# Optimization experiments

Measured on AMD Instinct MI355X. Metric: run time of the kernel, lower is better.

## Reference

```python
import jax, jax.numpy as jnp
import numpy as np

C_RATIO, T_RATIO = 0.8, 0.9

def _mlp(v, w1, w2):
    # v: [b, n]; w1: [hid, n]; w2: [n, hid]  (1x1x1 convs on pooled vector == matmuls)
    return jnp.einsum('nh,bh->bn', w2, jax.nn.relu(jnp.einsum('hn,bn->bh', w1, v)))

def _wta(x, ratio):
    # winner-take-all along last dim: keep top ceil(ratio*n) entries, zero the rest
    k = int(np.ceil(ratio * x.shape[-1]))
    thr = jax.lax.top_k(x, k)[0][..., -1:]
    mask = (x >= thr).astype(x.dtype)
    return x * mask, mask

def setup_inputs() -> dict:
    key = jax.random.key(0)
    ks = jax.random.split(key, 5)
    b, f, c, h, w = 16, 8, 256, 32, 32
    x = jax.random.normal(ks[0], (b, f, c, h, w), jnp.float32)
    ta_w1 = jax.random.normal(ks[1], (f, f), jnp.float32) * 0.3   # TimeAttention conv1 (reduction=1)
    ta_w2 = jax.random.normal(ks[2], (f, f), jnp.float32) * 0.3   # TimeAttention conv2
    ca_w1 = jax.random.normal(ks[3], (c, c), jnp.float32) * 0.06  # ChannelAttention conv1
    ca_w2 = jax.random.normal(ks[4], (c, c), jnp.float32) * 0.06  # ChannelAttention conv2
    return {"x": x, "ta_w1": ta_w1, "ta_w2": ta_w2, "ca_w1": ca_w1, "ca_w2": ca_w2}

def reference(x, ta_w1, ta_w2, ca_w1, ca_w2):
    # TimeAttention: global avg/max pool over (c,h,w) -> [b,f], shared MLP, sigmoid
    t_avg = x.mean(axis=(2, 3, 4))
    t_max = x.max(axis=(2, 3, 4))
    ta = jax.nn.sigmoid(_mlp(t_avg, ta_w1, ta_w2) + _mlp(t_max, ta_w1, ta_w2))  # [b,f]
    out = x * ta[:, :, None, None, None]
    # ChannelAttention on ta*x: pool over (f,h,w) -> [b,c]
    c_avg = out.mean(axis=(1, 3, 4))
    c_max = out.max(axis=(1, 3, 4))
    ca = jax.nn.sigmoid(_mlp(c_avg, ca_w1, ca_w2) + _mlp(c_max, ca_w1, ca_w2))  # [b,c]
    # winner-take-all saliency masking
    sal_c, mask_c = _wta(ca, C_RATIO)   # [b,c]
    sal_t, mask_t = _wta(ta, T_RATIO)   # [b,f]
    coef = (sal_t[:, :, None] * sal_c[:, None, :])[..., None, None]   # [b,f,c,1,1]
    mask = (mask_t[:, :, None] * mask_c[:, None, :])[..., None, None]
    return x * mask * coef
```

## Files before the change

kernel.cpp:

```cpp
#include <hip/hip_runtime.h>
#include <math.h>

#define B 16
#define F 8
#define C 256
#define HW 1024
#define NROWS (B*F*C)
#define KC 205

typedef float f4 __attribute__((ext_vector_type(4)));

__global__ __launch_bounds__(256) void k_rowstat(const float* __restrict__ x,
                                                 float* __restrict__ sums,
                                                 float* __restrict__ maxs) {
    const int wave = threadIdx.x >> 6;
    const int lane = threadIdx.x & 63;
    const int row  = blockIdx.x * 4 + wave;
    const float* p = x + (size_t)row * HW;

    float s = 0.f, m = -INFINITY;
#pragma unroll
    for (int k = 0; k < 4; ++k) {
        float4 v = *reinterpret_cast<const float4*>(p + k * 256 + lane * 4);
        s += (v.x + v.y) + (v.z + v.w);
        m = fmaxf(m, fmaxf(fmaxf(v.x, v.y), fmaxf(v.z, v.w)));
    }
#pragma unroll
    for (int off = 32; off > 0; off >>= 1) {
        s += __shfl_down(s, off);
        m = fmaxf(m, __shfl_down(m, off));
    }
    if (lane == 0) { sums[row] = s; maxs[row] = m; }
}

__global__ __launch_bounds__(256) void k_att(const float* __restrict__ sums,
                                             const float* __restrict__ maxs,
                                             const float* __restrict__ tw1,
                                             const float* __restrict__ tw2,
                                             const float* __restrict__ w1,
                                             const float* __restrict__ w2,
                                             float* __restrict__ srow) {
    __shared__ float tavg[F], tmx[F], th[F], ta_s[F];
    __shared__ float vavg[C], vmax[C], hsum[C], ca[C];
    const int b    = blockIdx.x;
    const int t    = threadIdx.x;
    const int wave = t >> 6;
    const int lane = t & 63;

    for (int f = wave; f < F; f += 4) {
        const float* sp = sums + (b * F + f) * C;
        const float* mp = maxs + (b * F + f) * C;
        float s = (sp[lane] + sp[lane + 64]) + (sp[lane + 128] + sp[lane + 192]);
        float m = fmaxf(fmaxf(mp[lane], mp[lane + 64]),
                        fmaxf(mp[lane + 128], mp[lane + 192]));
#pragma unroll
        for (int off = 32; off > 0; off >>= 1) {
            s += __shfl_down(s, off);
            m = fmaxf(m, __shfl_down(m, off));
        }
        if (lane == 0) { tavg[f] = s * (1.f / (float)(C * HW)); tmx[f] = m; }
    }
    __syncthreads();

    if (t < F) {
        float ha = 0.f, hm = 0.f;
        for (int n = 0; n < F; ++n) {
            float w = tw1[t * F + n];
            ha += w * tavg[n];
            hm += w * tmx[n];
        }
        th[t] = fmaxf(ha, 0.f) + fmaxf(hm, 0.f);
    }
    __syncthreads();
    if (t < F) {
        float o = 0.f;
        for (int h = 0; h < F; ++h) o += tw2[t * F + h] * th[h];
        ta_s[t] = 1.f / (1.f + expf(-o));
    }
    __syncthreads();

    {
        float s = 0.f, m = -INFINITY;
        for (int f = 0; f < F; ++f) {
            float w = ta_s[f];
            s += w * sums[(b * F + f) * C + t];
            m = fmaxf(m, w * maxs[(b * F + f) * C + t]);
        }
        vavg[t] = s * (1.f / (float)(F * HW));
        vmax[t] = m;
    }
    __syncthreads();

    {
        float ha = 0.f, hm = 0.f;
        const float* w1r = w1 + t * C;
        for (int n = 0; n < C; ++n) {
            float w = w1r[n];
            ha += w * vavg[n];
            hm += w * vmax[n];
        }
        hsum[t] = fmaxf(ha, 0.f) + fmaxf(hm, 0.f);
    }
    __syncthreads();

    float cav;
    {
        float o = 0.f;
        const float* w2r = w2 + t * C;
        for (int h = 0; h < C; ++h) o += w2r[h] * hsum[h];
        cav = 1.f / (1.f + expf(-o));
        ca[t] = cav;
    }
    __syncthreads();

    int rank = 0;
    for (int j = 0; j < C; ++j) rank += (ca[j] > cav);
    float sc = (rank < KC) ? cav : 0.f;
    for (int f = 0; f < F; ++f)
        srow[b * (F * C) + f * C + t] = ta_s[f] * sc;
}

__global__ __launch_bounds__(256) void k_scale(const float* __restrict__ x,
                                               const float* __restrict__ srow,
                                               float* __restrict__ out,
                                               int n4) {
    int idx = blockIdx.x * blockDim.x + threadIdx.x;
    const int stride = gridDim.x * blockDim.x;
    for (int i = idx; i < n4; i += stride) {
        f4 v = reinterpret_cast<const f4*>(x)[i];
        float sc = srow[i >> 8];
        v *= sc;
        __builtin_nontemporal_store(v, reinterpret_cast<f4*>(out) + i);
    }
}

extern "C" void kernel_launch(void* const* d_in, const int* in_sizes, int n_in,
                              void* d_out, int out_size, void* d_ws, size_t ws_size,
                              hipStream_t stream) {
    const float* x     = (const float*)d_in[0];
    const float* ta_w1 = (const float*)d_in[1];
    const float* ta_w2 = (const float*)d_in[2];
    const float* ca_w1 = (const float*)d_in[3];
    const float* ca_w2 = (const float*)d_in[4];
    float* out = (float*)d_out;

    float* ws   = (float*)d_ws;
    float* sums = ws;
    float* maxs = ws + NROWS;
    float* srow = ws + 2 * NROWS;

    k_rowstat<<<NROWS / 4, 256, 0, stream>>>(x, sums, maxs);
    k_att<<<B, 256, 0, stream>>>(sums, maxs, ta_w1, ta_w2, ca_w1, ca_w2, srow);
    k_scale<<<2048, 256, 0, stream>>>(x, srow, out, NROWS * HW / 4);
}
```

Baseline: 86.45 us.

## Fuse attention computation into scale kernel and skip loads for masked channels

The attention MLP kernel is merged into the scaling pass. Each of the 2048 blocks recomputes its batch's time and channel attention redundantly and then scales a 16-row chunk, which removes one launch and the srow round trip. Rows whose channel coefficient is zero are written as zeros without reading x, which saves about 20% of the read traffic. The row-stat kernel now has each wave reduce two rows with all eight loads issued up front. In exchange, every block repeats the 256x256 MLP and the O(C^2) ranking, which adds compute ahead of the streaming work.

```diff
diff --git a/kernel.cpp b/kernel.cpp
--- a/kernel.cpp
+++ b/kernel.cpp
@@ -15,37 +15,60 @@
                                                  float* __restrict__ maxs) {
     const int wave = threadIdx.x >> 6;
     const int lane = threadIdx.x & 63;
-    const int row  = blockIdx.x * 4 + wave;
-    const float* p = x + (size_t)row * HW;
+    const int row0 = blockIdx.x * 8 + wave * 2;
+    const float* p0 = x + (size_t)row0 * HW + lane * 4;
+    const float* p1 = p0 + HW;
 
-    float s = 0.f, m = -INFINITY;
-#pragma unroll
-    for (int k = 0; k < 4; ++k) {
-        float4 v = *reinterpret_cast<const float4*>(p + k * 256 + lane * 4);
-        s += (v.x + v.y) + (v.z + v.w);
-        m = fmaxf(m, fmaxf(fmaxf(v.x, v.y), fmaxf(v.z, v.w)));
-    }
+    float4 a0 = *reinterpret_cast<const float4*>(p0);
+    float4 a1 = *reinterpret_cast<const float4*>(p0 + 256);
+    float4 a2 = *reinterpret_cast<const float4*>(p0 + 512);
+    float4 a3 = *reinterpret_cast<const float4*>(p0 + 768);
+    float4 b0 = *reinterpret_cast<const float4*>(p1);
+    float4 b1 = *reinterpret_cast<const float4*>(p1 + 256);
+    float4 b2 = *reinterpret_cast<const float4*>(p1 + 512);
+    float4 b3 = *reinterpret_cast<const float4*>(p1 + 768);
+
+    float s0 = (((a0.x + a0.y) + (a0.z + a0.w)) + ((a1.x + a1.y) + (a1.z + a1.w)))
+             + (((a2.x + a2.y) + (a2.z + a2.w)) + ((a3.x + a3.y) + (a3.z + a3.w)));
+    float m0 = fmaxf(fmaxf(fmaxf(fmaxf(a0.x, a0.y), fmaxf(a0.z, a0.w)),
+                           fmaxf(fmaxf(a1.x, a1.y), fmaxf(a1.z, a1.w))),
+                     fmaxf(fmaxf(fmaxf(a2.x, a2.y), fmaxf(a2.z, a2.w)),
+                           fmaxf(fmaxf(a3.x, a3.y), fmaxf(a3.z, a3.w))));
+    float s1 = (((b0.x + b0.y) + (b0.z + b0.w)) + ((b1.x + b1.y) + (b1.z + b1.w)))
+             + (((b2.x + b2.y) + (b2.z + b2.w)) + ((b3.x + b3.y) + (b3.z + b3.w)));
+    float m1 = fmaxf(fmaxf(fmaxf(fmaxf(b0.x, b0.y), fmaxf(b0.z, b0.w)),
+                           fmaxf(fmaxf(b1.x, b1.y), fmaxf(b1.z, b1.w))),
+                     fmaxf(fmaxf(fmaxf(b2.x, b2.y), fmaxf(b2.z, b2.w)),
+                           fmaxf(fmaxf(b3.x, b3.y), fmaxf(b3.z, b3.w))));
+
 #pragma unroll
     for (int off = 32; off > 0; off >>= 1) {
-        s += __shfl_down(s, off);
-        m = fmaxf(m, __shfl_down(m, off));
+        s0 += __shfl_down(s0, off);
+        m0 = fmaxf(m0, __shfl_down(m0, off));
+        s1 += __shfl_down(s1, off);
+        m1 = fmaxf(m1, __shfl_down(m1, off));
     }
-    if (lane == 0) { sums[row] = s; maxs[row] = m; }
+    if (lane == 0) {
+        sums[row0] = s0; maxs[row0] = m0;
+        sums[row0 + 1] = s1; maxs[row0 + 1] = m1;
+    }
 }
 
-__global__ __launch_bounds__(256) void k_att(const float* __restrict__ sums,
-                                             const float* __restrict__ maxs,
-                                             const float* __restrict__ tw1,
-                                             const float* __restrict__ tw2,
-                                             const float* __restrict__ w1,
-                                             const float* __restrict__ w2,
-                                             float* __restrict__ srow) {
+__global__ __launch_bounds__(256) void k_att_scale(const float* __restrict__ x,
+                                                   const float* __restrict__ sums,
+                                                   const float* __restrict__ maxs,
+                                                   const float* __restrict__ tw1,
+                                                   const float* __restrict__ tw2,
+                                                   const float* __restrict__ w1,
+                                                   const float* __restrict__ w2,
+                                                   float* __restrict__ out) {
     __shared__ float tavg[F], tmx[F], th[F], ta_s[F];
-    __shared__ float vavg[C], vmax[C], hsum[C], ca[C];
-    const int b    = blockIdx.x;
-    const int t    = threadIdx.x;
-    const int wave = t >> 6;
-    const int lane = t & 63;
+    __shared__ float vavg[C], vmax[C], hsum[C], ca[C], sc_s[C];
+    const int b     = blockIdx.x >> 7;
+    const int chunk = blockIdx.x & 127;
+    const int t     = threadIdx.x;
+    const int wave  = t >> 6;
+    const int lane  = t & 63;
 
     for (int f = wave; f < F; f += 4) {
         const float* sp = sums + (b * F + f) * C;
@@ -113,24 +136,30 @@
     }
     __syncthreads();
 
-    int rank = 0;
-    for (int j = 0; j < C; ++j) rank += (ca[j] > cav);
-    float sc = (rank < KC) ? cav : 0.f;
-    for (int f = 0; f < F; ++f)
-        srow[b * (F * C) + f * C + t] = ta_s[f] * sc;
-}
+    {
+        int rank = 0;
+        for (int j = 0; j < C; ++j) rank += (ca[j] > cav);
+        sc_s[t] = (rank < KC) ? cav : 0.f;
+    }
+    __syncthreads();
 
-__global__ __launch_bounds__(256) void k_scale(const float* __restrict__ x,
-                                               const float* __restrict__ srow,
-                                               float* __restrict__ out,
-                                               int n4) {
-    int idx = blockIdx.x * blockDim.x + threadIdx.x;
-    const int stride = gridDim.x * blockDim.x;
-    for (int i = idx; i < n4; i += stride) {
-        f4 v = reinterpret_cast<const f4*>(x)[i];
-        float sc = srow[i >> 8];
-        v *= sc;
-        __builtin_nontemporal_store(v, reinterpret_cast<f4*>(out) + i);
+    const float taf = ta_s[chunk >> 4];
+    const int   c0  = (chunk & 15) * 16;
+    const int base4 = (b * 2048 + chunk * 16) * 256;
+    const f4* x4 = reinterpret_cast<const f4*>(x);
+    f4* o4 = reinterpret_cast<f4*>(out);
+
+    for (int it = 0; it < 16; ++it) {
+        const float scv = sc_s[c0 + it];
+        const int gi = base4 + it * 256 + t;
+        if (scv == 0.f) {
+            f4 z = {0.f, 0.f, 0.f, 0.f};
+            __builtin_nontemporal_store(z, o4 + gi);
+        } else {
+            f4 v = x4[gi];
+            v *= (taf * scv);
+            __builtin_nontemporal_store(v, o4 + gi);
+        }
     }
 }
 
@@ -147,9 +176,8 @@
     float* ws   = (float*)d_ws;
     float* sums = ws;
     float* maxs = ws + NROWS;
-    float* srow = ws + 2 * NROWS;
 
-    k_rowstat<<<NROWS / 4, 256, 0, stream>>>(x, sums, maxs);
-    k_att<<<B, 256, 0, stream>>>(sums, maxs, ta_w1, ta_w2, ca_w1, ca_w2, srow);
-    k_scale<<<2048, 256, 0, stream>>>(x, srow, out, NROWS * HW / 4);
+    k_rowstat<<<NROWS / 8, 256, 0, stream>>>(x, sums, maxs);
+    k_att_scale<<<B * 128, 256, 0, stream>>>(x, sums, maxs,
+                                             ta_w1, ta_w2, ca_w1, ca_w2, out);
 }
```

New measurement: 159.6 us. 1.85x slower.
